# Kernel tuning notes

Hardware: AMD Instinct MI355X
Metric: run time of the kernel (lower is better)

The kernel has to match this reference:

```python
import jax, jax.numpy as jnp
import numpy as np

COMMITMENT_COST = 0.25

def setup_inputs() -> dict:
    key = jax.random.key(0)
    k1, k2 = jax.random.split(key)
    inputs = jax.random.normal(k1, (32, 64, 64, 64), dtype=jnp.float32)  # [B, C=D, H, W]
    K, D = 512, 64
    # torch init: uniform(-1/K, 1/K)
    weight = jax.random.uniform(k2, (K, D), dtype=jnp.float32, minval=-1.0 / K, maxval=1.0 / K)
    return {"inputs": inputs, "weight": weight}

def reference(inputs, weight):
    B, C, H, W = inputs.shape
    x = jnp.transpose(inputs, (0, 2, 3, 1))  # [B, H, W, C]
    flat = x.reshape(-1, C)  # [N, D]
    # squared euclidean distances [N, K]
    d = (jnp.sum(flat ** 2, axis=1, keepdims=True)
         + jnp.sum(weight ** 2, axis=1)
         - 2.0 * flat @ weight.T)
    idx = jnp.argmin(d, axis=1)  # [N]
    quantized = weight[idx]  # gather == one-hot @ weight, [N, D]
    e_latent_loss = jnp.mean((jax.lax.stop_gradient(quantized) - flat) ** 2)
    q_latent_loss = jnp.mean((quantized - jax.lax.stop_gradient(flat)) ** 2)
    loss = q_latent_loss + COMMITMENT_COST * e_latent_loss
    # straight-through estimator
    q_st = flat + jax.lax.stop_gradient(quantized - flat)
    out = jnp.transpose(q_st.reshape(B, H, W, C), (0, 3, 1, 2))  # back to NCHW
    return out, loss
```

## Files before the change

### kernel.cpp

```cpp
#include <hip/hip_runtime.h>

typedef __attribute__((ext_vector_type(8))) __bf16 bf16x8;
typedef __attribute__((ext_vector_type(8))) unsigned short ushort8;
typedef __attribute__((ext_vector_type(4))) float floatx4;
typedef __attribute__((ext_vector_type(16))) float floatx16;

__device__ __forceinline__ unsigned short f2bf(float f) {
    unsigned int u = __builtin_bit_cast(unsigned int, f);
    unsigned int r = u + 0x7FFFu + ((u >> 16) & 1u);
    return (unsigned short)(r >> 16);
}
__device__ __forceinline__ float bf2f(unsigned short h) {
    return __builtin_bit_cast(float, ((unsigned int)h) << 16);
}

__global__ void vq_prep(const float* __restrict__ w, unsigned short* __restrict__ wext) {
    const int t = threadIdx.x;
    const int row = blockIdx.x * 4 + (t >> 6);
    const int c = t & 63;
    float v = w[row * 64 + c];
    wext[row * 80 + c] = f2bf(-2.f * v);
    float s = v * v;
#pragma unroll
    for (int off = 32; off; off >>= 1) s += __shfl_xor(s, off, 64);
    if (c == 0) {
        const unsigned short hi = f2bf(s);
        wext[row * 80 + 64] = hi;
        wext[row * 80 + 65] = f2bf(s - bf2f(hi));
    }
    if (c >= 2 && c < 16) wext[row * 80 + 64 + c] = 0;
}

__global__ void __launch_bounds__(256) vq_main(
    const float* __restrict__ in,
    const float* __restrict__ w,
    const unsigned short* __restrict__ wext,
    float* __restrict__ out,
    float* __restrict__ partials) {
    __shared__ unsigned short xs[2][2048];
    __shared__ float red[4][32];
    __shared__ float ws4[4];

    const int t = threadIdx.x;
    const int lane = t & 63;
    const int wv = t >> 6;
    const int bid = blockIdx.x;
    const int col = lane & 31;
    const int hi = lane >> 5;

    bf16x8 A[4][5];
#pragma unroll
    for (int i = 0; i < 4; ++i) {
        const int row = (wv * 4 + i) * 32 + col;
#pragma unroll
        for (int ch = 0; ch < 5; ++ch)
            A[i][ch] = *(const bf16x8*)&wext[row * 80 + ch * 16 + hi * 8];
    }
    ushort8 b4u = {0, 0, 0, 0, 0, 0, 0, 0};
    if (hi == 0) { b4u[0] = 0x3F80; b4u[1] = 0x3F80; }
    const bf16x8 Bf4 = __builtin_bit_cast(bf16x8, b4u);

    float x2acc = 0.f;
    float smin_acc = 0.f;

    {
        const int gt = bid * 4;
        const float* in_base = in + ((size_t)(gt >> 7) * 64) * 4096 + ((gt & 127) << 5);
#pragma unroll
        for (int it = 0; it < 2; ++it) {
            const int task = t + 256 * it;
            const int c = task >> 3, q = task & 7, p0 = q * 4;
            floatx4 v = *(const floatx4*)(in_base + (size_t)c * 4096 + p0);
            x2acc += v[0] * v[0] + v[1] * v[1] + v[2] * v[2] + v[3] * v[3];
            unsigned short* p = &xs[0][((c >> 3) * 32 + p0) * 8 + (c & 7)];
            p[0] = f2bf(v[0]); p[8] = f2bf(v[1]); p[16] = f2bf(v[2]); p[24] = f2bf(v[3]);
        }
    }
    __syncthreads();

#pragma unroll
    for (int ti = 0; ti < 4; ++ti) {
        const int cur = ti & 1;
        const int gt = bid * 4 + ti;

        bf16x8 Bf[4];
#pragma unroll
        for (int ch = 0; ch < 4; ++ch)
            Bf[ch] = *(const bf16x8*)&xs[cur][((2 * ch + hi) * 32 + col) * 8];

        if (ti < 3) {
            const int gn = gt + 1;
            const float* in_base = in + ((size_t)(gn >> 7) * 64) * 4096 + ((gn & 127) << 5);
#pragma unroll
            for (int it = 0; it < 2; ++it) {
                const int task = t + 256 * it;
                const int c = task >> 3, q = task & 7, p0 = q * 4;
                floatx4 v = *(const floatx4*)(in_base + (size_t)c * 4096 + p0);
                x2acc += v[0] * v[0] + v[1] * v[1] + v[2] * v[2] + v[3] * v[3];
                unsigned short* p = &xs[cur ^ 1][((c >> 3) * 32 + p0) * 8 + (c & 7)];
                p[0] = f2bf(v[0]); p[8] = f2bf(v[1]); p[16] = f2bf(v[2]); p[24] = f2bf(v[3]);
            }
        }

        float best = 1e30f;
#pragma unroll
        for (int i = 0; i < 4; ++i) {
            floatx16 acc = {0.f, 0.f, 0.f, 0.f, 0.f, 0.f, 0.f, 0.f,
                            0.f, 0.f, 0.f, 0.f, 0.f, 0.f, 0.f, 0.f};
            acc = __builtin_amdgcn_mfma_f32_32x32x16_bf16(A[i][0], Bf[0], acc, 0, 0, 0);
            acc = __builtin_amdgcn_mfma_f32_32x32x16_bf16(A[i][1], Bf[1], acc, 0, 0, 0);
            acc = __builtin_amdgcn_mfma_f32_32x32x16_bf16(A[i][2], Bf[2], acc, 0, 0, 0);
            acc = __builtin_amdgcn_mfma_f32_32x32x16_bf16(A[i][3], Bf[3], acc, 0, 0, 0);
            acc = __builtin_amdgcn_mfma_f32_32x32x16_bf16(A[i][4], Bf4,   acc, 0, 0, 0);
            const int code_base = (wv * 4 + i) * 32;
            float pk[16];
#pragma unroll
            for (int q = 0; q < 4; ++q) {
#pragma unroll
                for (int rr = 0; rr < 4; ++rr) {
                    const int r = q * 4 + rr;
                    const unsigned int code = (unsigned int)(code_base + 8 * q + 4 * hi + rr);
                    pk[r] = __builtin_bit_cast(float,
                        (__builtin_bit_cast(unsigned int, acc[r]) & 0xFFFFFE00u) | code);
                }
            }
#pragma unroll
            for (int s2 = 8; s2 >= 1; s2 >>= 1)
#pragma unroll
                for (int r = 0; r < s2; ++r) pk[r] = fminf(pk[r], pk[r + s2]);
            best = fminf(best, pk[0]);
        }
        best = fminf(best, __shfl_xor(best, 32, 64));
        if (lane < 32) red[wv][col] = best;
        __syncthreads();

        const float v = fminf(fminf(red[0][col], red[1][col]),
                              fminf(red[2][col], red[3][col]));
        if (wv == 0 && lane < 32)
            smin_acc += __builtin_bit_cast(float,
                __builtin_bit_cast(unsigned int, v) & 0xFFFFFE00u);

        float* out_base = out + ((size_t)(gt >> 7) * 64) * 4096 + ((gt & 127) << 5);
#pragma unroll
        for (int it = 0; it < 2; ++it) {
            const int task = t + 256 * it;
            const int c = task >> 3, q = task & 7, p0 = q * 4;
            floatx4 qv;
#pragma unroll
            for (int r = 0; r < 4; ++r) {
                const float pk = __shfl(v, p0 + r, 64);
                const int idx = (int)(__builtin_bit_cast(unsigned int, pk) & 511u);
                qv[r] = w[idx * 64 + c];
            }
            *(floatx4*)(out_base + (size_t)c * 4096 + p0) = qv;
        }
        __syncthreads();
    }

    float tot = x2acc + ((wv == 0 && lane < 32) ? smin_acc : 0.f);
#pragma unroll
    for (int off = 1; off < 64; off <<= 1) tot += __shfl_xor(tot, off, 64);
    if (lane == 0) ws4[wv] = tot;
    __syncthreads();
    if (t == 0) partials[bid] = ws4[0] + ws4[1] + ws4[2] + ws4[3];
}

__global__ void vq_reduce(const float* __restrict__ partials, float* __restrict__ loss) {
    const int t = threadIdx.x;
    float s = partials[t] + partials[t + 256] + partials[t + 512] + partials[t + 768];
#pragma unroll
    for (int off = 32; off; off >>= 1) s += __shfl_xor(s, off, 64);
    __shared__ float ws4[4];
    if ((t & 63) == 0) ws4[t >> 6] = s;
    __syncthreads();
    if (t == 0) loss[0] = (ws4[0] + ws4[1] + ws4[2] + ws4[3]) * (1.25f / 8388608.f);
}

extern "C" void kernel_launch(void* const* d_in, const int* in_sizes, int n_in,
                              void* d_out, int out_size, void* d_ws, size_t ws_size,
                              hipStream_t stream) {
    const float* in = (const float*)d_in[0];
    const float* w  = (const float*)d_in[1];
    float* out = (float*)d_out;
    float* loss = out + 8388608;
    unsigned short* wext = (unsigned short*)d_ws;
    float* partials = (float*)((char*)d_ws + 512 * 80 * 2);

    vq_prep<<<128, 256, 0, stream>>>(w, wext);
    vq_main<<<1024, 256, 0, stream>>>(in, w, wext, out, partials);
    vq_reduce<<<1, 256, 0, stream>>>(partials, loss);
}
```

Baseline: 104.2 us.

## Split argmin and codebook gather into separate kernels via index buffer

The fused kernel is split in two. The first kernel computes only the nearest-code indices and loss partials, writing 16-bit indices to a workspace buffer. The second kernel gathers codebook rows into shared memory and writes the NCHW output with a transposed, coalesced store pattern. The aim is to take the scattered gather and shuffle work out of the MFMA loop and lighten its register and sync pressure. The cost is an extra launch and a small index round-trip through global memory.

```diff
diff --git a/kernel.cpp b/kernel.cpp
--- a/kernel.cpp
+++ b/kernel.cpp
@@ -31,11 +31,10 @@
     if (c >= 2 && c < 16) wext[row * 80 + 64 + c] = 0;
 }
 
-__global__ void __launch_bounds__(256) vq_main(
+__global__ void __launch_bounds__(256) vq_argmin(
     const float* __restrict__ in,
-    const float* __restrict__ w,
     const unsigned short* __restrict__ wext,
-    float* __restrict__ out,
+    unsigned short* __restrict__ idxout,
     float* __restrict__ partials) {
     __shared__ unsigned short xs[2][2048];
     __shared__ float red[4][32];
@@ -134,25 +133,13 @@
         if (lane < 32) red[wv][col] = best;
         __syncthreads();
 
-        const float v = fminf(fminf(red[0][col], red[1][col]),
-                              fminf(red[2][col], red[3][col]));
-        if (wv == 0 && lane < 32)
+        if (wv == 0 && lane < 32) {
+            const float v = fminf(fminf(red[0][col], red[1][col]),
+                                  fminf(red[2][col], red[3][col]));
             smin_acc += __builtin_bit_cast(float,
                 __builtin_bit_cast(unsigned int, v) & 0xFFFFFE00u);
-
-        float* out_base = out + ((size_t)(gt >> 7) * 64) * 4096 + ((gt & 127) << 5);
-#pragma unroll
-        for (int it = 0; it < 2; ++it) {
-            const int task = t + 256 * it;
-            const int c = task >> 3, q = task & 7, p0 = q * 4;
-            floatx4 qv;
-#pragma unroll
-            for (int r = 0; r < 4; ++r) {
-                const float pk = __shfl(v, p0 + r, 64);
-                const int idx = (int)(__builtin_bit_cast(unsigned int, pk) & 511u);
-                qv[r] = w[idx * 64 + c];
-            }
-            *(floatx4*)(out_base + (size_t)c * 4096 + p0) = qv;
+            idxout[gt * 32 + col] =
+                (unsigned short)(__builtin_bit_cast(unsigned int, v) & 511u);
         }
         __syncthreads();
     }
@@ -163,6 +150,42 @@
     if (lane == 0) ws4[wv] = tot;
     __syncthreads();
     if (t == 0) partials[bid] = ws4[0] + ws4[1] + ws4[2] + ws4[3];
+}
+
+__global__ void __launch_bounds__(256) vq_gather(
+    const unsigned short* __restrict__ idx,
+    const float* __restrict__ w,
+    float* __restrict__ out) {
+    __shared__ float g[128][65];
+    __shared__ unsigned short idxs[128];
+
+    const int t = threadIdx.x;
+    const int bid = blockIdx.x;
+    const int b = bid >> 5;
+    const int p0 = (bid & 31) << 7;
+
+    if (t < 128) idxs[t] = idx[b * 4096 + p0 + t];
+    __syncthreads();
+
+    const int c0 = (t & 15) * 4;
+    const int rsub = t >> 4;
+#pragma unroll
+    for (int pass = 0; pass < 8; ++pass) {
+        const int r = pass * 16 + rsub;
+        const int code = idxs[r];
+        *(floatx4*)&g[r][c0] = *(const floatx4*)(w + code * 64 + c0);
+    }
+    __syncthreads();
+
+    const int c = t >> 2;
+    const int q = t & 3;
+    float* ob = out + ((size_t)b * 64 + c) * 4096 + p0 + q * 32;
+#pragma unroll
+    for (int k = 0; k < 8; ++k) {
+        const int p = q * 32 + k * 4;
+        floatx4 v = {g[p][c], g[p + 1][c], g[p + 2][c], g[p + 3][c]};
+        *(floatx4*)(ob + k * 4) = v;
+    }
 }
 
 __global__ void vq_reduce(const float* __restrict__ partials, float* __restrict__ loss) {
@@ -184,9 +207,11 @@
     float* out = (float*)d_out;
     float* loss = out + 8388608;
     unsigned short* wext = (unsigned short*)d_ws;
-    float* partials = (float*)((char*)d_ws + 512 * 80 * 2);
+    float* partials = (float*)((char*)d_ws + 81920);
+    unsigned short* idxbuf = (unsigned short*)((char*)d_ws + 86016);
 
     vq_prep<<<128, 256, 0, stream>>>(w, wext);
-    vq_main<<<1024, 256, 0, stream>>>(in, w, wext, out, partials);
+    vq_argmin<<<1024, 256, 0, stream>>>(in, wext, idxbuf, partials);
+    vq_gather<<<1024, 256, 0, stream>>>(idxbuf, w, out);
     vq_reduce<<<1, 256, 0, stream>>>(partials, loss);
 }
```

After: 110.1 us. +5.6%, slower.
